# Performance work log

Hardware: AMD Instinct MI355X
Metric: run time of the kernel (lower is better)

The kernel has to match this reference:

```python
import jax, jax.numpy as jnp
import numpy as np

GAMMA = 0.01
INFER_STEP = 4
C, B, G, S, L = 8, 32, 2048, 32, 3


def softor(x, axis, gamma=GAMMA):
    # gamma-weighted soft-or: gamma * logsumexp(x/gamma); renormalize if max > 1
    lse = gamma * jax.nn.logsumexp(x / gamma, axis=axis)
    m = jnp.max(lse)
    return jnp.where(m > 1.0, lse / m, lse)


def clause_fn(I_i, x):
    # I_i: [G, S, L] int indices into atom axis; x: [B, G]
    gathered = jnp.take(x, I_i, axis=1)        # [B, G, S, L]
    body = jnp.prod(gathered, axis=3)          # [B, G, S] (AND over body literals)
    return softor(body, axis=2)                # [B, G]   (OR over substitutions)


def setup_inputs() -> dict:
    key = jax.random.key(0)
    k1, k2 = jax.random.split(key)
    x = jax.random.uniform(k1, (B, G), dtype=jnp.float32)
    I = jax.random.randint(k2, (C, G, S, L), 0, G)
    return {"x": x, "I": I}


def reference(x, I):
    # R: [C, B, G] per-clause valuations, initialized from x
    R = jnp.broadcast_to(x[None], (C, B, G))
    r = jax.vmap(clause_fn)  # map over clause axis of I and R
    for _ in range(INFER_STEP):
        R = softor(jnp.stack([R, r(I, R)], axis=1), axis=1)
    return R
```

## Files before the change

kernel.cpp:

```cpp
#include <hip/hip_runtime.h>
#include <hip/hip_bf16.h>

#define C_ 8
#define B_ 32
#define G_ 2048
#define S_ 32
#define L_ 3
#define GB_ (G_ * B_)


#define OFF_BUF0 0
#define OFF_BUF1 524288
#define OFF_MAX  1048576
#define OFF_GMAX (OFF_MAX + 512)
#define ZERO_FLOATS 576

#define K_SCALE 144.26950408889634f
#define GLN2 0.0069314718055994531f

#define EXP2F(x) __builtin_amdgcn_exp2f(x)
#define LOG2F(x) __builtin_amdgcn_logf(x)

__device__ __forceinline__ void atomicMaxPos(float* a, float v) {
    atomicMax((unsigned*)a, __float_as_uint(v));
}

__device__ __forceinline__ float4 body3(float4 a, float4 b, float4 c) {
    float4 r;
    r.x = a.x * b.x * (c.x * K_SCALE);
    r.y = a.y * b.y * (c.y * K_SCALE);
    r.z = a.z * b.z * (c.z * K_SCALE);
    r.w = a.w * b.w * (c.w * K_SCALE);
    return r;
}
__device__ __forceinline__ float4 fmax4v(float4 a, float4 b) {
    float4 r;
    r.x = fmaxf(a.x, b.x); r.y = fmaxf(a.y, b.y);
    r.z = fmaxf(a.z, b.z); r.w = fmaxf(a.w, b.w);
    return r;
}
__device__ __forceinline__ float4 exp2m(float4 a, float4 m) {
    float4 r;
    r.x = EXP2F(a.x - m.x); r.y = EXP2F(a.y - m.y);
    r.z = EXP2F(a.z - m.z); r.w = EXP2F(a.w - m.w);
    return r;
}

__global__ __launch_bounds__(256, 2) void k_clause(const float* __restrict__ Rbase,
                                                   int xmode,
                                                   const int* __restrict__ I,
                                                   float* __restrict__ r_out,
                                                   const float* __restrict__ gmax_prev,
                                                   float* __restrict__ cmax_step) {
    __shared__ float sR[G_ * 4];
    __shared__ float sRed[4];

    const int tid = threadIdx.x;
    const int bid = blockIdx.x;
    const int c = bid >> 6;
    const int bh = (bid >> 3) & 7;
    const int gs = bid & 7;

    const float gm = gmax_prev ? gmax_prev[0] : 0.0f;
    const float sc = (gm > 1.0f) ? (1.0f / gm) : 1.0f;

    if (xmode) {
        const int j = tid >> 6;
        const int g0 = tid & 63;
        const float* xr = Rbase + (bh * 4 + j) * G_;
#pragma unroll
        for (int k = 0; k < 32; ++k) {
            const int g = g0 + 64 * k;
            sR[g * 4 + j] = xr[g];
        }
    } else {
        const float4* src = (const float4*)(Rbase + c * GB_ + bh * (G_ * 4));
        float4* dst = (float4*)sR;
#pragma unroll
        for (int k = 0; k < 8; ++k) {
            float4 v = src[tid + k * 256];
            v.x *= sc; v.y *= sc; v.z *= sc; v.w *= sc;
            dst[tid + k * 256] = v;
        }
    }
    __syncthreads();

    const float4* sR4 = (const float4*)sR;
    const int row = gs * 256 + tid;
    const int4* p = (const int4*)(I + (c * G_ + row) * 96);

    float4 lm[8], pp[8];
#pragma unroll
    for (int ch = 0; ch < 8; ++ch) {
        const int4 qa = p[ch * 3 + 0], qb = p[ch * 3 + 1], qc = p[ch * 3 + 2];
        const float4 b0 = body3(sR4[qa.x], sR4[qa.y], sR4[qa.z]);
        const float4 b1 = body3(sR4[qa.w], sR4[qb.x], sR4[qb.y]);
        const float4 b2 = body3(sR4[qb.z], sR4[qb.w], sR4[qc.x]);
        const float4 b3 = body3(sR4[qc.y], sR4[qc.z], sR4[qc.w]);
        const float4 l = fmax4v(fmax4v(b0, b1), fmax4v(b2, b3));
        const float4 e0 = exp2m(b0, l), e1 = exp2m(b1, l);
        const float4 e2 = exp2m(b2, l), e3 = exp2m(b3, l);
        float4 s;
        s.x = e0.x + e1.x + e2.x + e3.x;
        s.y = e0.y + e1.y + e2.y + e3.y;
        s.z = e0.z + e1.z + e2.z + e3.z;
        s.w = e0.w + e1.w + e2.w + e3.w;
        lm[ch] = l; pp[ch] = s;
    }
    float4 M = fmax4v(fmax4v(fmax4v(lm[0], lm[1]), fmax4v(lm[2], lm[3])),
                      fmax4v(fmax4v(lm[4], lm[5]), fmax4v(lm[6], lm[7])));
    float4 sum = make_float4(0.f, 0.f, 0.f, 0.f);
#pragma unroll
    for (int ch = 0; ch < 8; ++ch) {
        const float4 w = exp2m(lm[ch], M);
        sum.x += pp[ch].x * w.x; sum.y += pp[ch].y * w.y;
        sum.z += pp[ch].z * w.z; sum.w += pp[ch].w * w.w;
    }
    float4 lse;
    lse.x = GLN2 * (M.x + LOG2F(sum.x));
    lse.y = GLN2 * (M.y + LOG2F(sum.y));
    lse.z = GLN2 * (M.z + LOG2F(sum.z));
    lse.w = GLN2 * (M.w + LOG2F(sum.w));

    *(float4*)(r_out + ((c * 8 + bh) * G_ + row) * 4) = lse;

    float m = fmaxf(fmaxf(lse.x, lse.y), fmaxf(lse.z, lse.w));
#pragma unroll
    for (int o = 32; o; o >>= 1) m = fmaxf(m, __shfl_xor(m, o, 64));
    const int lane = tid & 63, wv = tid >> 6;
    if (lane == 0) sRed[wv] = m;
    __syncthreads();
    if (tid == 0) {
        float a = fmaxf(fmaxf(sRed[0], sRed[1]), fmaxf(sRed[2], sRed[3]));
        atomicMaxPos(&cmax_step[c * 16], a);
    }
}

__global__ __launch_bounds__(256, 8) void k_combine(const float* __restrict__ Rold,
                                                    int xmode,
                                                    const float* __restrict__ r_in,
                                                    float* __restrict__ Rnew,
                                                    const float* __restrict__ gmax_prev,
                                                    const float* __restrict__ cmax_step,
                                                    float* __restrict__ gmax_out) {
    __shared__ float sRed[4];
    const int tid = threadIdx.x;
    const int i4 = (blockIdx.x * 256 + tid) * 4;
    const int c = i4 >> 16;

    const float gm = gmax_prev ? gmax_prev[0] : 0.0f;
    const float sc = (gm > 1.0f) ? (1.0f / gm) : 1.0f;
    const float cmv = cmax_step[c * 16];
    const float scr = (cmv > 1.0f) ? (1.0f / cmv) : 1.0f;

    float4 Ro;
    if (xmode) {
        const int w = i4 & (GB_ - 1);
        const int bq = w >> 13;
        const int g = (w & 8191) >> 2;
        Ro.x = Rold[(bq * 4 + 0) * G_ + g];
        Ro.y = Rold[(bq * 4 + 1) * G_ + g];
        Ro.z = Rold[(bq * 4 + 2) * G_ + g];
        Ro.w = Rold[(bq * 4 + 3) * G_ + g];
    } else {
        Ro = *(const float4*)(Rold + i4);
    }
    const float4 rv = *(const float4*)(r_in + i4);
    float4 o;
    {
        float Rn = Ro.x * sc, rn = rv.x * scr;
        float M = fmaxf(Rn, rn), mn = fminf(Rn, rn);
        o.x = M + 0.01f * __logf(1.0f + __expf((mn - M) * 100.0f));
    }
    {
        float Rn = Ro.y * sc, rn = rv.y * scr;
        float M = fmaxf(Rn, rn), mn = fminf(Rn, rn);
        o.y = M + 0.01f * __logf(1.0f + __expf((mn - M) * 100.0f));
    }
    {
        float Rn = Ro.z * sc, rn = rv.z * scr;
        float M = fmaxf(Rn, rn), mn = fminf(Rn, rn);
        o.z = M + 0.01f * __logf(1.0f + __expf((mn - M) * 100.0f));
    }
    {
        float Rn = Ro.w * sc, rn = rv.w * scr;
        float M = fmaxf(Rn, rn), mn = fminf(Rn, rn);
        o.w = M + 0.01f * __logf(1.0f + __expf((mn - M) * 100.0f));
    }
    *(float4*)(Rnew + i4) = o;

    float mm = fmaxf(fmaxf(o.x, o.y), fmaxf(o.z, o.w));
#pragma unroll
    for (int off = 32; off; off >>= 1) mm = fmaxf(mm, __shfl_xor(mm, off, 64));
    const int lane = tid & 63, wv = tid >> 6;
    if (lane == 0) sRed[wv] = mm;
    __syncthreads();
    if (tid == 0) {
        float a = fmaxf(fmaxf(sRed[0], sRed[1]), fmaxf(sRed[2], sRed[3]));
        atomicMaxPos(gmax_out, a);
    }
}

__global__ __launch_bounds__(256) void k_out(const float* __restrict__ buf0,
                                             const float* __restrict__ gmaxslot,
                                             float* __restrict__ out) {
    __shared__ float sT[32 * 65];
    const int bid = blockIdx.x;
    const int c = bid >> 5;
    const int g0 = (bid & 31) << 6;
    const int tid = threadIdx.x;

    const float gm = gmaxslot[0];
    const float sc = (gm > 1.0f) ? (1.0f / gm) : 1.0f;

    const int r = tid >> 2, w = tid & 3;
#pragma unroll
    for (int k = 0; k < 8; ++k) {
        sT[(k * 4 + w) * 65 + r] = buf0[((c * 8 + k) * G_ + g0 + r) * 4 + w] * sc;
    }
    __syncthreads();
#pragma unroll
    for (int k = 0; k < 8; ++k) {
        const int j = tid + k * 256;
        const int b = j >> 6, gg = j & 63;
        out[(c * B_ + b) * G_ + g0 + gg] = sT[b * 65 + gg];
    }
}

extern "C" void kernel_launch(void* const* d_in, const int* in_sizes, int n_in,
                              void* d_out, int out_size, void* d_ws, size_t ws_size,
                              hipStream_t stream) {
    const float* x = (const float*)d_in[0];
    const int* I = (const int*)d_in[1];
    float* out = (float*)d_out;
    float* ws = (float*)d_ws;

    float* buf0 = ws + OFF_BUF0;
    float* buf1 = ws + OFF_BUF1;
    float* maxs = ws + OFF_MAX;
    float* gmax = ws + OFF_GMAX;

    hipMemsetAsync(ws + OFF_MAX, 0, ZERO_FLOATS * sizeof(float), stream);

    for (int t = 0; t < 4; ++t) {
        const float* Rsrc = (t == 0) ? x : buf0;
        const int xmode = (t == 0) ? 1 : 0;
        const float* gprev = (t == 0) ? nullptr : (gmax + (t - 1) * 16);
        float* cstep = maxs + t * 128;

        k_clause<<<512, 256, 0, stream>>>(Rsrc, xmode, I, buf1, gprev, cstep);
        k_combine<<<512, 256, 0, stream>>>(Rsrc, xmode, buf1, buf0, gprev, cstep,
                                           gmax + t * 16);
    }

    k_out<<<256, 256, 0, stream>>>(buf0, gmax + 48, out);
}
```

Measured before the change: 94.44 us.

## Fuse clause and combine into one cooperative kernel with grid-wide atomic barrier

```diff
diff --git a/kernel.cpp b/kernel.cpp
--- a/kernel.cpp
+++ b/kernel.cpp
@@ -10,10 +10,10 @@
 
 
 #define OFF_BUF0 0
-#define OFF_BUF1 524288
 #define OFF_MAX  1048576
 #define OFF_GMAX (OFF_MAX + 512)
-#define ZERO_FLOATS 576
+#define OFF_DONE (OFF_MAX + 576)
+#define ZERO_FLOATS 640
 
 #define K_SCALE 144.26950408889634f
 #define GLN2 0.0069314718055994531f
@@ -45,15 +45,22 @@
     r.z = EXP2F(a.z - m.z); r.w = EXP2F(a.w - m.w);
     return r;
 }
-
-__global__ __launch_bounds__(256, 2) void k_clause(const float* __restrict__ Rbase,
-                                                   int xmode,
-                                                   const int* __restrict__ I,
-                                                   float* __restrict__ r_out,
-                                                   const float* __restrict__ gmax_prev,
-                                                   float* __restrict__ cmax_step) {
+__device__ __forceinline__ float softor2(float Rn, float rn) {
+    const float M = fmaxf(Rn, rn), mn = fminf(Rn, rn);
+    return M + 0.01f * __logf(1.0f + __expf((mn - M) * 100.0f));
+}
+
+__global__ __launch_bounds__(256, 2) void k_step(const float* __restrict__ Rbase,
+                                                 int xmode,
+                                                 const int* __restrict__ I,
+                                                 float* __restrict__ Rnew,
+                                                 const float* __restrict__ gmax_prev,
+                                                 float* __restrict__ cmax_step,
+                                                 float* __restrict__ gmax_out,
+                                                 unsigned* __restrict__ done_slot) {
     __shared__ float sR[G_ * 4];
     __shared__ float sRed[4];
+    __shared__ float sCmv;
 
     const int tid = threadIdx.x;
     const int bid = blockIdx.x;
@@ -122,8 +129,6 @@
     lse.z = GLN2 * (M.z + LOG2F(sum.z));
     lse.w = GLN2 * (M.w + LOG2F(sum.w));
 
-    *(float4*)(r_out + ((c * 8 + bh) * G_ + row) * 4) = lse;
-
     float m = fmaxf(fmaxf(lse.x, lse.y), fmaxf(lse.z, lse.w));
 #pragma unroll
     for (int o = 32; o; o >>= 1) m = fmaxf(m, __shfl_xor(m, o, 64));
@@ -133,66 +138,31 @@
     if (tid == 0) {
         float a = fmaxf(fmaxf(sRed[0], sRed[1]), fmaxf(sRed[2], sRed[3]));
         atomicMaxPos(&cmax_step[c * 16], a);
-    }
-}
-
-__global__ __launch_bounds__(256, 8) void k_combine(const float* __restrict__ Rold,
-                                                    int xmode,
-                                                    const float* __restrict__ r_in,
-                                                    float* __restrict__ Rnew,
-                                                    const float* __restrict__ gmax_prev,
-                                                    const float* __restrict__ cmax_step,
-                                                    float* __restrict__ gmax_out) {
-    __shared__ float sRed[4];
-    const int tid = threadIdx.x;
-    const int i4 = (blockIdx.x * 256 + tid) * 4;
-    const int c = i4 >> 16;
-
-    const float gm = gmax_prev ? gmax_prev[0] : 0.0f;
-    const float sc = (gm > 1.0f) ? (1.0f / gm) : 1.0f;
-    const float cmv = cmax_step[c * 16];
+        __threadfence();
+        atomicAdd(done_slot, 1u);
+        while (__hip_atomic_load(done_slot, __ATOMIC_RELAXED,
+                                 __HIP_MEMORY_SCOPE_AGENT) < 512u)
+            __builtin_amdgcn_s_sleep(1);
+        const unsigned cu = __hip_atomic_load((const unsigned*)&cmax_step[c * 16],
+                                              __ATOMIC_RELAXED,
+                                              __HIP_MEMORY_SCOPE_AGENT);
+        sCmv = __uint_as_float(cu);
+    }
+    __syncthreads();
+
+    const float cmv = sCmv;
     const float scr = (cmv > 1.0f) ? (1.0f / cmv) : 1.0f;
-
-    float4 Ro;
-    if (xmode) {
-        const int w = i4 & (GB_ - 1);
-        const int bq = w >> 13;
-        const int g = (w & 8191) >> 2;
-        Ro.x = Rold[(bq * 4 + 0) * G_ + g];
-        Ro.y = Rold[(bq * 4 + 1) * G_ + g];
-        Ro.z = Rold[(bq * 4 + 2) * G_ + g];
-        Ro.w = Rold[(bq * 4 + 3) * G_ + g];
-    } else {
-        Ro = *(const float4*)(Rold + i4);
-    }
-    const float4 rv = *(const float4*)(r_in + i4);
+    const float4 Ro = sR4[row];
     float4 o;
-    {
-        float Rn = Ro.x * sc, rn = rv.x * scr;
-        float M = fmaxf(Rn, rn), mn = fminf(Rn, rn);
-        o.x = M + 0.01f * __logf(1.0f + __expf((mn - M) * 100.0f));
-    }
-    {
-        float Rn = Ro.y * sc, rn = rv.y * scr;
-        float M = fmaxf(Rn, rn), mn = fminf(Rn, rn);
-        o.y = M + 0.01f * __logf(1.0f + __expf((mn - M) * 100.0f));
-    }
-    {
-        float Rn = Ro.z * sc, rn = rv.z * scr;
-        float M = fmaxf(Rn, rn), mn = fminf(Rn, rn);
-        o.z = M + 0.01f * __logf(1.0f + __expf((mn - M) * 100.0f));
-    }
-    {
-        float Rn = Ro.w * sc, rn = rv.w * scr;
-        float M = fmaxf(Rn, rn), mn = fminf(Rn, rn);
-        o.w = M + 0.01f * __logf(1.0f + __expf((mn - M) * 100.0f));
-    }
-    *(float4*)(Rnew + i4) = o;
+    o.x = softor2(Ro.x, lse.x * scr);
+    o.y = softor2(Ro.y, lse.y * scr);
+    o.z = softor2(Ro.z, lse.z * scr);
+    o.w = softor2(Ro.w, lse.w * scr);
+    *(float4*)(Rnew + ((c * 8 + bh) * G_ + row) * 4) = o;
 
     float mm = fmaxf(fmaxf(o.x, o.y), fmaxf(o.z, o.w));
 #pragma unroll
     for (int off = 32; off; off >>= 1) mm = fmaxf(mm, __shfl_xor(mm, off, 64));
-    const int lane = tid & 63, wv = tid >> 6;
     if (lane == 0) sRed[wv] = mm;
     __syncthreads();
     if (tid == 0) {
@@ -236,21 +206,24 @@
     float* ws = (float*)d_ws;
 
     float* buf0 = ws + OFF_BUF0;
-    float* buf1 = ws + OFF_BUF1;
     float* maxs = ws + OFF_MAX;
     float* gmax = ws + OFF_GMAX;
+    unsigned* done = (unsigned*)(ws + OFF_DONE);
 
     hipMemsetAsync(ws + OFF_MAX, 0, ZERO_FLOATS * sizeof(float), stream);
 
     for (int t = 0; t < 4; ++t) {
         const float* Rsrc = (t == 0) ? x : buf0;
-        const int xmode = (t == 0) ? 1 : 0;
+        int xmode = (t == 0) ? 1 : 0;
         const float* gprev = (t == 0) ? nullptr : (gmax + (t - 1) * 16);
         float* cstep = maxs + t * 128;
-
-        k_clause<<<512, 256, 0, stream>>>(Rsrc, xmode, I, buf1, gprev, cstep);
-        k_combine<<<512, 256, 0, stream>>>(Rsrc, xmode, buf1, buf0, gprev, cstep,
-                                           gmax + t * 16);
+        float* gout = gmax + t * 16;
+        unsigned* dslot = done + t * 16;
+
+        void* args[] = {(void*)&Rsrc, (void*)&xmode, (void*)&I, (void*)&buf0,
+                        (void*)&gprev, (void*)&cstep, (void*)&gout, (void*)&dslot};
+        hipLaunchCooperativeKernel((const void*)k_step, dim3(512), dim3(256),
+                                   args, 0, stream);
     }
 
     k_out<<<256, 256, 0, stream>>>(buf0, gmax + 48, out);
```

After: 273.0 us. +189.1%, slower.
